# Kernel optimization log

Measured on AMD Instinct MI355X. Metric: run time of the kernel, lower is better.

Reference implementation:

```python
import jax, jax.numpy as jnp
import numpy as np

B, T, C = 8, 2048, 1024
HS, HO = 64, 64  # head_size, head_output_dim

def setup_inputs() -> dict:
    key = jax.random.key(0)
    k1, k2, k3, k4 = jax.random.split(key, 4)
    x = jax.random.normal(k1, (B, T, C), dtype=jnp.float32)
    Wk = jax.random.normal(k2, (HS, C), dtype=jnp.float32) * (C ** -0.5)
    Wq = jax.random.normal(k3, (HS, C), dtype=jnp.float32) * (C ** -0.5)
    Wv = jax.random.normal(k4, (HO, C), dtype=jnp.float32) * (C ** -0.5)
    return {"x": x, "Wk": Wk, "Wq": Wq, "Wv": Wv}

def reference(x, Wk, Wq, Wv):
    Bx, Tx, Cx = x.shape
    k = jnp.einsum('btc,hc->bth', x, Wk)  # [B,T,HS]
    q = jnp.einsum('btc,hc->bth', x, Wq)  # [B,T,HS]
    v = jnp.einsum('btc,oc->bto', x, Wv)  # [B,T,HO]
    scores = jnp.einsum('bth,bsh->bts', q, k)  # [B,T,T]
    causal = jnp.tril(jnp.ones((Tx, Tx), dtype=bool))
    scores = jnp.where(causal, scores, -jnp.inf)
    # original scales AFTER masking; -inf * scale stays -inf, same softmax result
    weights = jax.nn.softmax(scores * (HS ** -0.5), axis=-1)
    return jnp.einsum('bts,bso->bto', weights, v)
```

## Files before the change

### kernel.cpp

```cpp
#include <hip/hip_runtime.h>
#include <hip/hip_bf16.h>

typedef __attribute__((ext_vector_type(8))) short short8;
typedef __attribute__((ext_vector_type(4))) float float4v;

#define LOG2E 1.44269504088896340736f

__device__ __forceinline__ unsigned short f2bf(float f) {
    unsigned int u = __float_as_uint(f);
    unsigned int r = (u + 0x7fffu + ((u >> 16) & 1u)) >> 16;
    return (unsigned short)r;
}

__global__ void wconv_kernel(const float* __restrict__ Wk, const float* __restrict__ Wq,
                             const float* __restrict__ Wv, unsigned short* __restrict__ Wb) {
    int i = blockIdx.x * 256 + threadIdx.x;
    if (i >= 192 * 1024) return;
    float v;
    if (i < 65536)       v = Wk[i];
    else if (i < 131072) v = Wq[i - 65536];
    else                 v = Wv[i - 131072];
    Wb[i] = f2bf(v);
}

__global__ __launch_bounds__(256) void proj_kernel(
    const float* __restrict__ x, const unsigned short* __restrict__ Wb,
    unsigned short* __restrict__ qs, unsigned short* __restrict__ ks,
    unsigned short* __restrict__ vT) {
    __shared__ unsigned short Bl[2][192 * 72];

    const int tid  = threadIdx.x;
    const int lane = tid & 63;
    const int wave = tid >> 6;
    const int rg   = wave & 1;
    const int g    = wave >> 1;
    const int quad = lane >> 4;
    const int l16  = lane & 15;
    const int t0   = blockIdx.x * 32;

    const int srow = tid >> 3;
    const int scol = (tid & 7) * 8;

    const int rowA = t0 + rg * 16 + l16;
    const float* xr = x + (size_t)rowA * 1024;

    float4v acc[6];
#pragma unroll
    for (int n = 0; n < 6; n++) acc[n] = (float4v){0.f, 0.f, 0.f, 0.f};

    short8 breg[6];
#pragma unroll
    for (int i = 0; i < 6; i++)
        breg[i] = *(const short8*)(Wb + (size_t)(i * 32 + srow) * 1024 + scol);
    float4v areg[4];
    areg[0] = *(const float4v*)(xr + quad * 8);
    areg[1] = *(const float4v*)(xr + quad * 8 + 4);
    areg[2] = *(const float4v*)(xr + 32 + quad * 8);
    areg[3] = *(const float4v*)(xr + 32 + quad * 8 + 4);
#pragma unroll
    for (int i = 0; i < 6; i++)
        *(short8*)&Bl[0][(i * 32 + srow) * 72 + scol] = breg[i];
    __syncthreads();

#pragma unroll 2
    for (int kt = 0; kt < 16; kt++) {
        const int kn = ((kt + 1) & 15) * 64;
        short8 bnext[6];
#pragma unroll
        for (int i = 0; i < 6; i++)
            bnext[i] = *(const short8*)(Wb + (size_t)(i * 32 + srow) * 1024 + kn + scol);
        float4v anext[4];
        anext[0] = *(const float4v*)(xr + kn + quad * 8);
        anext[1] = *(const float4v*)(xr + kn + quad * 8 + 4);
        anext[2] = *(const float4v*)(xr + kn + 32 + quad * 8);
        anext[3] = *(const float4v*)(xr + kn + 32 + quad * 8 + 4);
        const unsigned short* Bc = Bl[kt & 1];
#pragma unroll
        for (int kc = 0; kc < 2; kc++) {
            short8 af;
#pragma unroll
            for (int j = 0; j < 4; j++) af[j] = (short)f2bf(areg[kc * 2][j]);
#pragma unroll
            for (int j = 0; j < 4; j++) af[4 + j] = (short)f2bf(areg[kc * 2 + 1][j]);
#pragma unroll
            for (int n = 0; n < 6; n++) {
                const short8 bf = *(const short8*)&Bc[((g * 6 + n) * 16 + l16) * 72 + kc * 32 + quad * 8];
                acc[n] = __builtin_amdgcn_mfma_f32_16x16x32_bf16(af, bf, acc[n], 0, 0, 0);
            }
        }
        unsigned short* Bn = (unsigned short*)Bl[(kt + 1) & 1];
#pragma unroll
        for (int i = 0; i < 6; i++)
            *(short8*)&Bn[(i * 32 + srow) * 72 + scol] = bnext[i];
        __syncthreads();
#pragma unroll
        for (int i = 0; i < 4; i++) areg[i] = anext[i];
    }

    const int rowD = t0 + rg * 16 + quad * 4;
#pragma unroll
    for (int r = 0; r < 4; r++) {
        const int t = rowD + r;
        const int b = t >> 11, tt = t & 2047;
        if (g == 0) {
#pragma unroll
            for (int n = 0; n < 4; n++)
                ks[(size_t)t * 64 + n * 16 + l16] = f2bf(acc[n][r]);
#pragma unroll
            for (int n = 4; n < 6; n++)
                qs[(size_t)t * 64 + (n - 4) * 16 + l16] = f2bf(acc[n][r] * 0.125f);
        } else {
#pragma unroll
            for (int n = 0; n < 2; n++)
                qs[(size_t)t * 64 + (n + 2) * 16 + l16] = f2bf(acc[n][r] * 0.125f);
#pragma unroll
            for (int n = 2; n < 6; n++)
                vT[(size_t)b * 131072 + (size_t)((n - 2) * 16 + l16) * 2048 + tt] = f2bf(acc[n][r]);
        }
    }
}

__global__ __launch_bounds__(256) void attn_kernel(
    const unsigned short* __restrict__ qs, const unsigned short* __restrict__ ks,
    const unsigned short* __restrict__ vT, float* __restrict__ out) {
    __shared__ unsigned short Kl[4 * 64 * 72];
    __shared__ unsigned short Vl[64 * 264];
    __shared__ unsigned short P[4][16 * 72];
    __shared__ float Ll[4][16];
    float* Of = (float*)Kl;

    const int tid  = threadIdx.x;
    const int lane = tid & 63;
    const int wave = tid >> 6;
    const int quad = lane >> 4;
    const int l16  = lane & 15;
    const int bx   = blockIdx.x;
    const int b    = bx & 7;
    const int i    = bx >> 3;
    const int qt   = (i & 1) ? (127 - (i >> 1)) : (i >> 1);
    const int t0   = qt * 16;

    const unsigned short* qb = qs + (size_t)b * 131072;
    const unsigned short* kb = ks + (size_t)b * 131072;
    const unsigned short* vb = vT + (size_t)b * 131072;

    const int ksr = tid >> 3;
    const int ksc = (tid & 7) * 8;
    const int vsr = tid >> 5;
    const int vsc = (tid & 31) * 8;

    const int qrow = t0 + l16;
    const short8 qf0 = *(const short8*)(qb + (size_t)qrow * 64 + quad * 8);
    const short8 qf1 = *(const short8*)(qb + (size_t)qrow * 64 + 32 + quad * 8);

    float4v o[4];
#pragma unroll
    for (int ot = 0; ot < 4; ot++) o[ot] = (float4v){0.f, 0.f, 0.f, 0.f};
    float lpart = 0.f;

    const int nkb  = (qt >> 2) + 1;
    const int nsup = (nkb + 3) >> 2;

    for (int s = 0; s < nsup; s++) {
        const int key0 = s * 256;
        __syncthreads();
#pragma unroll
        for (int i2 = 0; i2 < 8; i2++) {
            int kr = key0 + i2 * 32 + ksr; kr = kr < 2047 ? kr : 2047;
            *(short8*)&Kl[(i2 * 32 + ksr) * 72 + ksc] = *(const short8*)(kb + (size_t)kr * 64 + ksc);
        }
#pragma unroll
        for (int i2 = 0; i2 < 8; i2++) {
            const int orow = i2 * 8 + vsr;
            int kc2 = key0 + vsc; kc2 = kc2 < 2040 ? kc2 : 2040;
            *(short8*)&Vl[orow * 264 + vsc] = *(const short8*)(vb + (size_t)orow * 2048 + kc2);
        }
        __syncthreads();

        const int jt = s * 4 + wave;
        if (jt < nkb) {
            const int kbase = wave * 64;
            float4v sv[4];
#pragma unroll
            for (int kt = 0; kt < 4; kt++) {
                const short8 ka = *(const short8*)&Kl[(kbase + kt * 16 + l16) * 72 + quad * 8];
                const short8 kc = *(const short8*)&Kl[(kbase + kt * 16 + l16) * 72 + 32 + quad * 8];
                float4v z = (float4v){0.f, 0.f, 0.f, 0.f};
                z = __builtin_amdgcn_mfma_f32_16x16x32_bf16(ka, qf0, z, 0, 0, 0);
                sv[kt] = __builtin_amdgcn_mfma_f32_16x16x32_bf16(kc, qf1, z, 0, 0, 0);
            }
            if (jt == nkb - 1) {
#pragma unroll
                for (int kt = 0; kt < 4; kt++)
#pragma unroll
                    for (int r = 0; r < 4; r++)
                        if (jt * 64 + kt * 16 + quad * 4 + r > qrow) sv[kt][r] = -1e30f;
            }
#pragma unroll
            for (int kt = 0; kt < 4; kt++) {
                float p0 = exp2f(sv[kt][0] * LOG2E);
                float p1 = exp2f(sv[kt][1] * LOG2E);
                float p2 = exp2f(sv[kt][2] * LOG2E);
                float p3 = exp2f(sv[kt][3] * LOG2E);
                lpart += (p0 + p1) + (p2 + p3);
                unsigned int lo = (unsigned int)f2bf(p0) | ((unsigned int)f2bf(p1) << 16);
                unsigned int hi = (unsigned int)f2bf(p2) | ((unsigned int)f2bf(p3) << 16);
                unsigned long long w = ((unsigned long long)hi << 32) | lo;
                *(unsigned long long*)&P[wave][l16 * 72 + kt * 16 + quad * 4] = w;
            }
#pragma unroll
            for (int kc = 0; kc < 2; kc++) {
                const short8 pf = *(const short8*)&P[wave][l16 * 72 + kc * 32 + quad * 8];
#pragma unroll
                for (int ot = 0; ot < 4; ot++) {
                    const short8 vf = *(const short8*)&Vl[(ot * 16 + l16) * 264 + wave * 64 + kc * 32 + quad * 8];
                    o[ot] = __builtin_amdgcn_mfma_f32_16x16x32_bf16(pf, vf, o[ot], 0, 0, 0);
                }
            }
        }
    }

    lpart += __shfl_xor(lpart, 16);
    lpart += __shfl_xor(lpart, 32);
    __syncthreads();
#pragma unroll
    for (int r = 0; r < 4; r++)
#pragma unroll
        for (int ot = 0; ot < 4; ot++)
            Of[wave * 1088 + (quad * 4 + r) * 68 + ot * 16 + l16] = o[ot][r];
    if (lane < 16) Ll[wave][lane] = lpart;
    __syncthreads();

    {
        const int row = tid >> 4;
        const int c0  = (tid & 15) * 4;
        const float lsum = Ll[0][row] + Ll[1][row] + Ll[2][row] + Ll[3][row];
        float4v v0 = *(const float4v*)&Of[0 * 1088 + row * 68 + c0];
        float4v v1 = *(const float4v*)&Of[1 * 1088 + row * 68 + c0];
        float4v v2 = *(const float4v*)&Of[2 * 1088 + row * 68 + c0];
        float4v v3 = *(const float4v*)&Of[3 * 1088 + row * 68 + c0];
        float4v res;
        const float inv = 1.0f / lsum;
#pragma unroll
        for (int j = 0; j < 4; j++)
            res[j] = ((v0[j] + v1[j]) + (v2[j] + v3[j])) * inv;
        float* ob = out + (size_t)b * 131072 + (size_t)(t0 + row) * 64 + c0;
        *(float4v*)ob = res;
    }
}

extern "C" void kernel_launch(void* const* d_in, const int* in_sizes, int n_in,
                              void* d_out, int out_size, void* d_ws, size_t ws_size,
                              hipStream_t stream) {
    const float* x  = (const float*)d_in[0];
    const float* Wk = (const float*)d_in[1];
    const float* Wq = (const float*)d_in[2];
    const float* Wv = (const float*)d_in[3];
    float* out = (float*)d_out;

    unsigned short* Wb  = (unsigned short*)d_ws;
    unsigned short* qsb = (unsigned short*)((char*)d_ws + 393216);
    unsigned short* ksb = qsb + 1048576;
    unsigned short* vTb = ksb + 1048576;

    hipLaunchKernelGGL(wconv_kernel, dim3(768), dim3(256), 0, stream, Wk, Wq, Wv, Wb);
    hipLaunchKernelGGL(proj_kernel, dim3(512), dim3(256), 0, stream, x, Wb, qsb, ksb, vTb);
    hipLaunchKernelGGL(attn_kernel, dim3(1024), dim3(256), 0, stream, qsb, ksb, vTb, out);
}
```

Before: 152.4 us.

## Stage projection weight tiles directly into LDS with an XOR-swizzled layout

In the projection kernel, weight tiles now go straight from global memory into shared memory through global_load_lds. This replaces the old path of loading into registers and then writing to a padded shared-memory buffer. The shared layout changes from padded rows to 64-wide rows with an XOR swizzle on the column chunk, to avoid bank conflicts on the MFMA operand reads. The barrier moves to the top of the loop so one barrier per iteration covers the double buffering. This frees registers and removes the LDS store instructions, but correctness now depends on the compiler waiting for the asynchronous LDS writes before reads.

```diff
diff --git a/kernel.cpp b/kernel.cpp
--- a/kernel.cpp
+++ b/kernel.cpp
@@ -5,6 +5,9 @@
 typedef __attribute__((ext_vector_type(4))) float float4v;
 
 #define LOG2E 1.44269504088896340736f
+
+typedef __attribute__((address_space(1))) const unsigned int gu32;
+typedef __attribute__((address_space(3))) unsigned int su32;
 
 __device__ __forceinline__ unsigned short f2bf(float f) {
     unsigned int u = __float_as_uint(f);
@@ -27,7 +30,7 @@
     const float* __restrict__ x, const unsigned short* __restrict__ Wb,
     unsigned short* __restrict__ qs, unsigned short* __restrict__ ks,
     unsigned short* __restrict__ vT) {
-    __shared__ unsigned short Bl[2][192 * 72];
+    __shared__ unsigned short Bl[2][12288];
 
     const int tid  = threadIdx.x;
     const int lane = tid & 63;
@@ -38,8 +41,8 @@
     const int l16  = lane & 15;
     const int t0   = blockIdx.x * 32;
 
-    const int srow = tid >> 3;
-    const int scol = (tid & 7) * 8;
+    const int srow_in = lane >> 3;
+    const int csrc    = (lane & 7) ^ srow_in;
 
     const int rowA = t0 + rg * 16 + l16;
     const float* xr = x + (size_t)rowA * 1024;
@@ -48,27 +51,33 @@
 #pragma unroll
     for (int n = 0; n < 6; n++) acc[n] = (float4v){0.f, 0.f, 0.f, 0.f};
 
-    short8 breg[6];
-#pragma unroll
-    for (int i = 0; i < 6; i++)
-        breg[i] = *(const short8*)(Wb + (size_t)(i * 32 + srow) * 1024 + scol);
+#define STAGE_B(BUF, KN)                                                          \
+    {                                                                             \
+        _Pragma("unroll")                                                         \
+        for (int i = 0; i < 6; i++) {                                             \
+            const int region = wave * 6 + i;                                      \
+            const int rowg   = region * 8 + srow_in;                              \
+            const unsigned short* src = Wb + (size_t)rowg * 1024 + (KN) + csrc * 8; \
+            __builtin_amdgcn_global_load_lds((gu32*)src,                          \
+                                             (su32*)&Bl[BUF][region * 512],       \
+                                             16, 0, 0);                           \
+        }                                                                         \
+    }
+
+    STAGE_B(0, 0)
     float4v areg[4];
     areg[0] = *(const float4v*)(xr + quad * 8);
     areg[1] = *(const float4v*)(xr + quad * 8 + 4);
     areg[2] = *(const float4v*)(xr + 32 + quad * 8);
     areg[3] = *(const float4v*)(xr + 32 + quad * 8 + 4);
-#pragma unroll
-    for (int i = 0; i < 6; i++)
-        *(short8*)&Bl[0][(i * 32 + srow) * 72 + scol] = breg[i];
-    __syncthreads();
+
+    const int swz = l16 & 7;
 
 #pragma unroll 2
     for (int kt = 0; kt < 16; kt++) {
+        __syncthreads();
         const int kn = ((kt + 1) & 15) * 64;
-        short8 bnext[6];
-#pragma unroll
-        for (int i = 0; i < 6; i++)
-            bnext[i] = *(const short8*)(Wb + (size_t)(i * 32 + srow) * 1024 + kn + scol);
+        STAGE_B((kt + 1) & 1, kn)
         float4v anext[4];
         anext[0] = *(const float4v*)(xr + kn + quad * 8);
         anext[1] = *(const float4v*)(xr + kn + quad * 8 + 4);
@@ -84,18 +93,16 @@
             for (int j = 0; j < 4; j++) af[4 + j] = (short)f2bf(areg[kc * 2 + 1][j]);
 #pragma unroll
             for (int n = 0; n < 6; n++) {
-                const short8 bf = *(const short8*)&Bc[((g * 6 + n) * 16 + l16) * 72 + kc * 32 + quad * 8];
+                const int row  = (g * 6 + n) * 16 + l16;
+                const int coff = ((kc * 4 + quad) ^ swz) * 8;
+                const short8 bf = *(const short8*)&Bc[row * 64 + coff];
                 acc[n] = __builtin_amdgcn_mfma_f32_16x16x32_bf16(af, bf, acc[n], 0, 0, 0);
             }
         }
-        unsigned short* Bn = (unsigned short*)Bl[(kt + 1) & 1];
-#pragma unroll
-        for (int i = 0; i < 6; i++)
-            *(short8*)&Bn[(i * 32 + srow) * 72 + scol] = bnext[i];
-        __syncthreads();
 #pragma unroll
         for (int i = 0; i < 4; i++) areg[i] = anext[i];
     }
+#undef STAGE_B
 
     const int rowD = t0 + rg * 16 + quad * 4;
 #pragma unroll
```

Result: no change. 151.9 us (-0.3%).
